# Kernel optimization log

Hardware: AMD Instinct MI355X
Metric: run time of the kernel (lower is better)

The kernel has to match this reference:

```python
import jax, jax.numpy as jnp
import numpy as np

N_NODES = 100000
N_EDGES = 1600000
DIM = 128
N_LAYERS = 4


def setup_inputs() -> dict:
    key = jax.random.key(0)
    ks = jax.random.split(key, 6)
    h = jax.random.normal(ks[0], (N_NODES, DIM), dtype=jnp.float32)
    src = jax.random.randint(ks[1], (N_EDGES,), 0, N_NODES, dtype=jnp.int32)
    dst = jax.random.randint(ks[2], (N_EDGES,), 0, N_NODES, dtype=jnp.int32)
    scale = 1.0 / np.sqrt(DIM)
    W_embed = jax.random.normal(ks[3], (DIM, DIM), dtype=jnp.float32) * scale
    b_embed = jnp.zeros((DIM,), dtype=jnp.float32)
    Ws = jax.random.normal(ks[4], (N_LAYERS, DIM, DIM), dtype=jnp.float32) * scale
    bs = jnp.zeros((N_LAYERS, DIM), dtype=jnp.float32)
    return {"h": h, "src": src, "dst": dst, "W_embed": W_embed,
            "b_embed": b_embed, "Ws": Ws, "bs": bs}


def reference(h, src, dst, W_embed, b_embed, Ws, bs):
    # Symmetric GCN normalization (DGL GraphConv norm='both'):
    # out-degree on src side, in-degree on dst side, clamped to >= 1.
    ones = jnp.ones(src.shape, h.dtype)
    deg_out = jax.ops.segment_sum(ones, src, num_segments=N_NODES)
    deg_in = jax.ops.segment_sum(ones, dst, num_segments=N_NODES)
    norm_s = jax.lax.rsqrt(jnp.maximum(deg_out, 1.0))  # [N]
    norm_d = jax.lax.rsqrt(jnp.maximum(deg_in, 1.0))   # [N]

    # embedding_h (dropout p=0 -> identity)
    h = h @ W_embed + b_embed

    for i in range(N_LAYERS):
        h_in = h
        # gather -> scale -> scatter-add (A_norm @ h)
        m = h[src] * norm_s[src, None]                              # [E, D]
        agg = jax.ops.segment_sum(m, dst, num_segments=N_NODES)    # [N, D]
        z = (agg * norm_d[:, None]) @ Ws[i] + bs[i]                 # GraphConv weight+bias
        z = jax.nn.relu(z)                                          # activation
        h = h_in + z                                                # residual
    return h
```

## Files before the change

### kernel.cpp

```cpp
#include <hip/hip_runtime.h>

#define DIMN 128
#define NLAYERS 4
#define KP 136
#define WTSH (2 * DIMN * KP)

#define BQL 9
#define BUCKW 512
#define BUCKCAP 10240
#define BSCH 4096
#define NBUK_MAX 256

#define HP_P 3
#define HP_C 48
#define HIST_BLOCKS (HP_P * HP_C)
#define HW_WORDS 16667

typedef __attribute__((ext_vector_type(8))) short bf16x8;
typedef __attribute__((ext_vector_type(4))) float f32x4;

__device__ inline float bfu2f(unsigned int u) { return __uint_as_float(u << 16); }
__device__ inline unsigned short f2bf(float f) {
    unsigned int u = __float_as_uint(f);
    return (unsigned short)((u + 0x7fffu + ((u >> 16) & 1u)) >> 16);
}
__device__ inline float blo(unsigned int u) { return __uint_as_float(u << 16); }
__device__ inline float bhi(unsigned int u) { return __uint_as_float(u & 0xffff0000u); }

__global__ __launch_bounds__(256) void k_pre(const int* __restrict__ src,
                                             const float* __restrict__ We,
                                             const float* __restrict__ Wlayers,
                                             unsigned int* __restrict__ degOutP,
                                             short* __restrict__ wt, int N, int E) {
    __shared__ unsigned int hsm[HW_WORDS];
    int tid = threadIdx.x;
    int bid = blockIdx.x;

    if (bid < HIST_BLOCKS) {
        int c = bid / HP_P;
        int p = bid % HP_P;
        int W = (N + 1) / 2;
        int w0 = p * HW_WORDS;
        int wn = min(HW_WORDS, W - w0);
        if (wn <= 0) return;
        int per = ((E + HP_C - 1) / HP_C + 3) & ~3;
        int e0 = c * per;
        int e1 = min(e0 + per, E);
        if (e0 >= e1) {
            for (int i = tid; i < wn; i += 256) degOutP[(size_t)c * W + w0 + i] = 0u;
            return;
        }
        for (int i = tid; i < wn; i += 256) hsm[i] = 0u;
        __syncthreads();
        int nvec = (e1 - e0) >> 2;
        const int4* sv = (const int4*)(src + e0);
        for (int it = tid; it < nvec; it += 256) {
            int4 v = sv[it];
            int w;
            w = (v.x >> 1) - w0; if ((unsigned)w < (unsigned)wn) atomicAdd(&hsm[w], 1u << ((v.x & 1) << 4));
            w = (v.y >> 1) - w0; if ((unsigned)w < (unsigned)wn) atomicAdd(&hsm[w], 1u << ((v.y & 1) << 4));
            w = (v.z >> 1) - w0; if ((unsigned)w < (unsigned)wn) atomicAdd(&hsm[w], 1u << ((v.z & 1) << 4));
            w = (v.w >> 1) - w0; if ((unsigned)w < (unsigned)wn) atomicAdd(&hsm[w], 1u << ((v.w & 1) << 4));
        }
        for (int j = e0 + (nvec << 2) + tid; j < e1; j += 256) {
            int s = src[j];
            int w = (s >> 1) - w0;
            if ((unsigned)w < (unsigned)wn) atomicAdd(&hsm[w], 1u << ((s & 1) << 4));
        }
        __syncthreads();
        for (int i = tid; i < wn; i += 256) degOutP[(size_t)c * W + w0 + i] = hsm[i];
        return;
    }

    {
        int m = bid - HIST_BLOCKS;
        const float* Wm = (m == 0) ? We : Wlayers + (size_t)(m - 1) * DIMN * DIMN;
        short* o = wt + (size_t)m * WTSH;
#pragma unroll
        for (int it = 0; it < 16; ++it) {
            int f = it * 1024 + tid * 4;
            float4 v = *(const float4*)(Wm + f);
            int k = f >> 7, n = f & 127;
            float vv[4] = {v.x, v.y, v.z, v.w};
#pragma unroll
            for (int j = 0; j < 4; ++j) {
                unsigned short hb = f2bf(vv[j]);
                float lo = vv[j] - bfu2f(hb);
                o[(n + j) * KP + k] = (short)hb;
                o[DIMN * KP + (n + j) * KP + k] = (short)f2bf(lo);
            }
        }
    }
}

__global__ __launch_bounds__(256) void k_binsort(const int* __restrict__ src,
                                                 const int* __restrict__ dst,
                                                 int* __restrict__ gcur,
                                                 int2* __restrict__ pairs,
                                                 int E, int NBUK) {
    __shared__ int cnt[NBUK_MAX];
    __shared__ int bofs[NBUK_MAX];
    __shared__ int gof[NBUK_MAX];
    __shared__ int scan_s[256];
    __shared__ int2 stg[BSCH];
    int tid = threadIdx.x;
    int e0 = blockIdx.x * BSCH;
    int n = min(BSCH, E - e0);
    if (n <= 0) return;
    cnt[tid] = 0;
    __syncthreads();

    int nv = n >> 2;
    const int4* dv4 = (const int4*)(dst + e0);
    for (int it = tid; it < nv; it += 256) {
        int4 d = dv4[it];
        atomicAdd(&cnt[d.x >> BQL], 1);
        atomicAdd(&cnt[d.y >> BQL], 1);
        atomicAdd(&cnt[d.z >> BQL], 1);
        atomicAdd(&cnt[d.w >> BQL], 1);
    }
    for (int j = (nv << 2) + tid; j < n; j += 256) {
        atomicAdd(&cnt[dst[e0 + j] >> BQL], 1);
    }
    __syncthreads();

    int myc = cnt[tid];
    scan_s[tid] = myc;
    __syncthreads();
    for (int off = 1; off < 256; off <<= 1) {
        int x = scan_s[tid];
        if (tid >= off) x += scan_s[tid - off];
        __syncthreads();
        scan_s[tid] = x;
        __syncthreads();
    }
    bofs[tid] = scan_s[tid] - myc;
    gof[tid] = (myc > 0 && tid < NBUK) ? atomicAdd(&gcur[tid], myc) : 0;
    cnt[tid] = 0;
    __syncthreads();

    const int4* sv4 = (const int4*)(src + e0);
    for (int it = tid; it < nv; it += 256) {
        int4 d = dv4[it];
        int4 s = sv4[it];
        int b, p;
        b = d.x >> BQL; p = bofs[b] + atomicAdd(&cnt[b], 1); stg[p] = make_int2(s.x, d.x);
        b = d.y >> BQL; p = bofs[b] + atomicAdd(&cnt[b], 1); stg[p] = make_int2(s.y, d.y);
        b = d.z >> BQL; p = bofs[b] + atomicAdd(&cnt[b], 1); stg[p] = make_int2(s.z, d.z);
        b = d.w >> BQL; p = bofs[b] + atomicAdd(&cnt[b], 1); stg[p] = make_int2(s.w, d.w);
    }
    for (int j = (nv << 2) + tid; j < n; j += 256) {
        int d = dst[e0 + j], s = src[e0 + j];
        int b = d >> BQL;
        int p = bofs[b] + atomicAdd(&cnt[b], 1);
        stg[p] = make_int2(s, d);
    }
    __syncthreads();

    for (int i = tid; i < n; i += 256) {
        int2 pr = stg[i];
        int b = pr.y >> BQL;
        int go = gof[b] + (i - bofs[b]);
        if (go < BUCKCAP) pairs[(size_t)b * BUCKCAP + go] = pr;
    }
}

__global__ __launch_bounds__(256) void k_build(const int2* __restrict__ pairs,
                                               const int* __restrict__ gcur,
                                               int* __restrict__ csr,
                                               int* __restrict__ rowptr,
                                               int* __restrict__ deg, int N) {
    int b = blockIdx.x;
    int tid = threadIdx.x;
    int cntb = gcur[b];
    if (cntb > BUCKCAP) cntb = BUCKCAP;
    __shared__ int c[BUCKW];
    __shared__ int pf[BUCKW];
    c[tid] = 0; c[tid + 256] = 0;
    __syncthreads();
    const int2* bp = pairs + (size_t)b * BUCKCAP;
    for (int i = tid; i < cntb; i += 256) atomicAdd(&c[bp[i].y & (BUCKW - 1)], 1);
    __syncthreads();
    pf[tid] = c[tid]; pf[tid + 256] = c[tid + 256];
    __syncthreads();
    for (int off = 1; off < BUCKW; off <<= 1) {
        int i0 = tid, i1 = tid + 256;
        int v0 = pf[i0] + ((i0 >= off) ? pf[i0 - off] : 0);
        int v1 = pf[i1] + ((i1 >= off) ? pf[i1 - off] : 0);
        __syncthreads();
        pf[i0] = v0; pf[i1] = v1;
        __syncthreads();
    }
    {
        int i0 = tid, i1 = tid + 256;
        int c0 = c[i0], c1 = c[i1];
        int ex0 = pf[i0] - c0, ex1 = pf[i1] - c1;
        pf[i0] = ex0; pf[i1] = ex1;
        int gn0 = (b << BQL) + i0, gn1 = (b << BQL) + i1;
        if (gn0 < N) { rowptr[gn0] = b * BUCKCAP + ex0; deg[gn0] = c0; }
        if (gn1 < N) { rowptr[gn1] = b * BUCKCAP + ex1; deg[gn1] = c1; }
        c[i0] = 0; c[i1] = 0;
    }
    __syncthreads();
    int* cb = csr + (size_t)b * BUCKCAP;
    for (int i = tid; i < cntb; i += 256) {
        int2 p = bp[i];
        int ld = p.y & (BUCKW - 1);
        int pos = pf[ld] + atomicAdd(&c[ld], 1);
        cb[pos] = p.x;
    }
}

__global__ __launch_bounds__(256) void k_norms(const int* __restrict__ deg,
                                               const unsigned int* __restrict__ degOutP,
                                               float* __restrict__ norm_d,
                                               float* __restrict__ norm_s, int N) {
    int i = blockIdx.x * 256 + threadIdx.x;
    int W = (N + 1) / 2;
    if (i < W) {
        unsigned s0 = 0, s1 = 0;
#pragma unroll 8
        for (int c = 0; c < HP_C; ++c) {
            unsigned v = degOutP[(size_t)c * W + i];
            s0 += v & 0xffffu;
            s1 += v >> 16;
        }
        int n0 = 2 * i, n1 = 2 * i + 1;
        norm_s[n0] = rsqrtf(fmaxf((float)s0, 1.0f));
        norm_d[n0] = rsqrtf(fmaxf((float)deg[n0], 1.0f));
        if (n1 < N) {
            norm_s[n1] = rsqrtf(fmaxf((float)s1, 1.0f));
            norm_d[n1] = rsqrtf(fmaxf((float)deg[n1], 1.0f));
        }
    }
}

__global__ __launch_bounds__(256) void k_gemm_f32(const float* __restrict__ A,
                                                  const short* __restrict__ Wt,
                                                  const float* __restrict__ bg,
                                                  float* __restrict__ tgt,
                                                  const float* __restrict__ norm_s,
                                                  unsigned short* __restrict__ Hs, int N) {
    __shared__ short Wl[WTSH];
    __shared__ float bias_s[DIMN];
    int tid = threadIdx.x;
    {
        const uint4* g = (const uint4*)Wt;
        uint4* l = (uint4*)Wl;
#pragma unroll
        for (int it = 0; it < 17; ++it) {
            int ix = it * 256 + tid;
            if (ix < WTSH / 8) l[ix] = g[ix];
        }
        if (tid < DIMN) bias_s[tid] = bg[tid];
    }
    __syncthreads();

    int lane = tid & 63;
    int wv = tid >> 6;
    int quad = lane >> 4;
    int l15 = lane & 15;
    int row0 = blockIdx.x * 128 + wv * 32;

    f32x4 acc[2][8];
#pragma unroll
    for (int s = 0; s < 2; ++s)
#pragma unroll
        for (int ct = 0; ct < 8; ++ct) acc[s][ct] = (f32x4){0.f, 0.f, 0.f, 0.f};

    for (int ks = 0; ks < 4; ++ks) {
        int kb = ks * 32 + quad * 8;
        bf16x8 ah[2], al[2];
#pragma unroll
        for (int s = 0; s < 2; ++s) {
            int r = row0 + s * 16 + l15;
            if (r > N - 1) r = N - 1;
            const float* ap = A + (size_t)r * DIMN + kb;
            float4 p = *(const float4*)ap;
            float4 q = *(const float4*)(ap + 4);
            float fv[8] = {p.x, p.y, p.z, p.w, q.x, q.y, q.z, q.w};
#pragma unroll
            for (int j = 0; j < 8; ++j) {
                unsigned short hb = f2bf(fv[j]);
                ah[s][j] = (short)hb;
                al[s][j] = (short)f2bf(fv[j] - bfu2f(hb));
            }
        }
#pragma unroll
        for (int ct = 0; ct < 8; ++ct) {
            const short* bp = Wl + (ct * 16 + l15) * KP + kb;
            bf16x8 bh = *(const bf16x8*)bp;
            bf16x8 bl = *(const bf16x8*)(bp + DIMN * KP);
#pragma unroll
            for (int s = 0; s < 2; ++s) {
                acc[s][ct] = __builtin_amdgcn_mfma_f32_16x16x32_bf16(ah[s], bh, acc[s][ct], 0, 0, 0);
                acc[s][ct] = __builtin_amdgcn_mfma_f32_16x16x32_bf16(al[s], bh, acc[s][ct], 0, 0, 0);
                acc[s][ct] = __builtin_amdgcn_mfma_f32_16x16x32_bf16(ah[s], bl, acc[s][ct], 0, 0, 0);
            }
        }
    }

#pragma unroll
    for (int s = 0; s < 2; ++s) {
        int rbase = row0 + s * 16 + quad * 4;
        float ns[4];
#pragma unroll
        for (int rj = 0; rj < 4; ++rj) {
            int row = rbase + rj;
            ns[rj] = (row < N) ? norm_s[row] : 0.f;
        }
#pragma unroll
        for (int ct = 0; ct < 8; ++ct) {
            int col = ct * 16 + l15;
            float bv = bias_s[col];
#pragma unroll
            for (int rj = 0; rj < 4; ++rj) {
                int row = rbase + rj;
                if (row < N) {
                    float o = acc[s][ct][rj] + bv;
                    __builtin_nontemporal_store(o, &tgt[(size_t)row * DIMN + col]);
                    Hs[(size_t)row * DIMN + col] = f2bf(o * ns[rj]);
                }
            }
        }
    }
}

__global__ __launch_bounds__(256) void k_gemm_bf(const unsigned short* __restrict__ A,
                                                 const short* __restrict__ Wt,
                                                 const float* __restrict__ bg,
                                                 const float* __restrict__ Hres,
                                                 float* __restrict__ tgt,
                                                 const float* __restrict__ norm_s,
                                                 unsigned short* __restrict__ Hs, int N) {
    __shared__ short Wl[WTSH];
    __shared__ float bias_s[DIMN];
    int tid = threadIdx.x;
    {
        const uint4* g = (const uint4*)Wt;
        uint4* l = (uint4*)Wl;
#pragma unroll
        for (int it = 0; it < 17; ++it) {
            int ix = it * 256 + tid;
            if (ix < WTSH / 8) l[ix] = g[ix];
        }
        if (tid < DIMN) bias_s[tid] = bg[tid];
    }
    __syncthreads();

    int lane = tid & 63;
    int wv = tid >> 6;
    int quad = lane >> 4;
    int l15 = lane & 15;
    int row0 = blockIdx.x * 128 + wv * 32;

    f32x4 acc[2][8];
#pragma unroll
    for (int s = 0; s < 2; ++s)
#pragma unroll
        for (int ct = 0; ct < 8; ++ct) acc[s][ct] = (f32x4){0.f, 0.f, 0.f, 0.f};

    for (int ks = 0; ks < 4; ++ks) {
        int kb = ks * 32 + quad * 8;
        bf16x8 ah[2];
#pragma unroll
        for (int s = 0; s < 2; ++s) {
            int r = row0 + s * 16 + l15;
            if (r > N - 1) r = N - 1;
            ah[s] = *(const bf16x8*)(A + (size_t)r * DIMN + kb);
        }
#pragma unroll
        for (int ct = 0; ct < 8; ++ct) {
            const short* bp = Wl + (ct * 16 + l15) * KP + kb;
            bf16x8 bh = *(const bf16x8*)bp;
            bf16x8 bl = *(const bf16x8*)(bp + DIMN * KP);
#pragma unroll
            for (int s = 0; s < 2; ++s) {
                acc[s][ct] = __builtin_amdgcn_mfma_f32_16x16x32_bf16(ah[s], bh, acc[s][ct], 0, 0, 0);
                acc[s][ct] = __builtin_amdgcn_mfma_f32_16x16x32_bf16(ah[s], bl, acc[s][ct], 0, 0, 0);
            }
        }
    }

    bool doHs = (Hs != nullptr);
#pragma unroll
    for (int s = 0; s < 2; ++s) {
        int rbase = row0 + s * 16 + quad * 4;
        float ns[4];
        if (doHs) {
#pragma unroll
            for (int rj = 0; rj < 4; ++rj) {
                int row = rbase + rj;
                ns[rj] = (row < N) ? norm_s[row] : 0.f;
            }
        }
#pragma unroll
        for (int ct = 0; ct < 8; ++ct) {
            int col = ct * 16 + l15;
            float bv = bias_s[col];
#pragma unroll
            for (int rj = 0; rj < 4; ++rj) {
                int row = rbase + rj;
                if (row < N) {
                    float o = fmaxf(acc[s][ct][rj] + bv, 0.f) + Hres[(size_t)row * DIMN + col];
                    __builtin_nontemporal_store(o, &tgt[(size_t)row * DIMN + col]);
                    if (doHs) Hs[(size_t)row * DIMN + col] = f2bf(o * ns[rj]);
                }
            }
        }
    }
}

__global__ __launch_bounds__(256) void k_spmm(const unsigned int* __restrict__ Hs,
                                              unsigned short* __restrict__ AggB,
                                              const int* __restrict__ csr,
                                              const int* __restrict__ rowptr,
                                              const int* __restrict__ deg,
                                              const float* __restrict__ norm_d, int N) {
    int wave = (blockIdx.x * blockDim.x + threadIdx.x) >> 6;
    int lane = threadIdx.x & 63;
    if (wave >= N) return;
    int cnt = deg[wave];
    const int* base = csr + rowptr[wave];
    int g = lane >> 5;
    int l5 = lane & 31;
    const uint2* H2 = (const uint2*)Hs;
    float4 acc = make_float4(0.f, 0.f, 0.f, 0.f);

    int emain = cnt & ~7;
    int e = 0;
    for (; e < emain; e += 8) {
        int s0 = base[e + g];
        int s1 = base[e + 2 + g];
        int s2 = base[e + 4 + g];
        int s3 = base[e + 6 + g];
        uint2 h0 = H2[(size_t)s0 * 32 + l5];
        uint2 h1 = H2[(size_t)s1 * 32 + l5];
        uint2 h2 = H2[(size_t)s2 * 32 + l5];
        uint2 h3 = H2[(size_t)s3 * 32 + l5];
        acc.x += blo(h0.x); acc.y += bhi(h0.x);
        acc.z += blo(h0.y); acc.w += bhi(h0.y);
        acc.x += blo(h1.x); acc.y += bhi(h1.x);
        acc.z += blo(h1.y); acc.w += bhi(h1.y);
        acc.x += blo(h2.x); acc.y += bhi(h2.x);
        acc.z += blo(h2.y); acc.w += bhi(h2.y);
        acc.x += blo(h3.x); acc.y += bhi(h3.x);
        acc.z += blo(h3.y); acc.w += bhi(h3.y);
    }
    for (; e < cnt; e += 2) {
        int ee = e + g;
        int sc = base[min(ee, cnt - 1)];
        uint2 hv = H2[(size_t)sc * 32 + l5];
        if (ee < cnt) {
            acc.x += blo(hv.x); acc.y += bhi(hv.x);
            acc.z += blo(hv.y); acc.w += bhi(hv.y);
        }
    }
    acc.x += __shfl_xor(acc.x, 32);
    acc.y += __shfl_xor(acc.y, 32);
    acc.z += __shfl_xor(acc.z, 32);
    acc.w += __shfl_xor(acc.w, 32);
    if (g == 0) {
        float nd = norm_d[wave];
        unsigned long long p =
            (unsigned long long)((unsigned)f2bf(acc.x * nd) | ((unsigned)f2bf(acc.y * nd) << 16)) |
            ((unsigned long long)((unsigned)f2bf(acc.z * nd) | ((unsigned)f2bf(acc.w * nd) << 16)) << 32);
        __builtin_nontemporal_store(p, &((unsigned long long*)AggB)[(size_t)wave * 32 + l5]);
    }
}

static inline char* align256(char* p) {
    return (char*)(((uintptr_t)p + 255) & ~(uintptr_t)255);
}

extern "C" void kernel_launch(void* const* d_in, const int* in_sizes, int n_in,
                              void* d_out, int out_size, void* d_ws, size_t ws_size,
                              hipStream_t stream) {
    const float* h_in = (const float*)d_in[0];
    const int* src = (const int*)d_in[1];
    const int* dst = (const int*)d_in[2];
    const float* W_embed = (const float*)d_in[3];
    const float* b_embed = (const float*)d_in[4];
    const float* Ws = (const float*)d_in[5];
    const float* bs = (const float*)d_in[6];
    float* out = (float*)d_out;

    const int N = in_sizes[0] / DIMN;
    const int E = in_sizes[1];
    const int W = (N + 1) / 2;
    const int NBUK = (N + BUCKW - 1) >> BQL;

    char* w = (char*)d_ws;
    float* Hc = (float*)w;               w = align256(w + (size_t)N * DIMN * 4);
    unsigned short* AggB = (unsigned short*)w; w = align256(w + (size_t)N * DIMN * 2);
    unsigned short* Hs = (unsigned short*)w;   w = align256(w + (size_t)N * DIMN * 2);
    int2* pairs = (int2*)w;              w = align256(w + (size_t)NBUK * BUCKCAP * 8);
    int* csr = (int*)w;                  w = align256(w + (size_t)NBUK * BUCKCAP * 4);
    int* rowptr = (int*)w;               w = align256(w + (size_t)N * 4);
    int* deg = (int*)w;                  w = align256(w + (size_t)N * 4);
    int* gcur = (int*)w;                 w = align256(w + (size_t)NBUK * 4);
    unsigned int* degOutP = (unsigned int*)w;  w = align256(w + (size_t)HP_C * W * 4);
    float* norm_s = (float*)w;           w = align256(w + (size_t)N * 4);
    float* norm_d = (float*)w;           w = align256(w + (size_t)N * 4);
    short* wt = (short*)w;               w = align256(w + (size_t)5 * WTSH * 2);

    (void)hipMemsetAsync(gcur, 0, (size_t)NBUK * 4, stream);

    int gb = (N + 127) / 128;
    int nb = (W + 255) / 256;
    int bb = (E + BSCH - 1) / BSCH;

    k_pre<<<HIST_BLOCKS + 5, 256, 0, stream>>>(src, W_embed, Ws, degOutP, wt, N, E);

    k_binsort<<<bb, 256, 0, stream>>>(src, dst, gcur, pairs, E, NBUK);
    k_build<<<NBUK, 256, 0, stream>>>(pairs, gcur, csr, rowptr, deg, N);

    k_norms<<<nb, 256, 0, stream>>>(deg, degOutP, norm_d, norm_s, N);

    k_gemm_f32<<<gb, 256, 0, stream>>>(h_in, wt, b_embed, Hc, norm_s, Hs, N);

    int sb = (N + 3) / 4;
    for (int l = 0; l < NLAYERS; ++l) {
        k_spmm<<<sb, 256, 0, stream>>>((const unsigned int*)Hs, AggB, csr, rowptr, deg, norm_d, N);
        float* tgt = (l == NLAYERS - 1) ? out : Hc;
        unsigned short* hs_next = (l == NLAYERS - 1) ? (unsigned short*)nullptr : Hs;
        k_gemm_bf<<<gb, 256, 0, stream>>>(AggB, wt + (size_t)(l + 1) * WTSH,
                                          bs + (size_t)l * DIMN, Hc, tgt, norm_s, hs_next, N);
    }
}
```

Before: 711.2 us.

## Read weights from global, stage GEMM epilogue through LDS for vectorized stores

The GEMM kernels no longer copy the split-bf16 weight matrices into shared memory; they read B fragments directly from global/L2 using an unpadded layout. The epilogue writes accumulators into a per-wave LDS buffer, then each lane writes a full row segment with float4 and uint4 stores, replacing scattered scalar stores. Launch bounds now request 4 blocks per SM, and the SpMM output store drops the nontemporal hint. The aim is to cut the per-block weight-staging cost and improve store coalescing. The risks are extra L2 traffic for weight reads, plus added block-level barriers in the epilogue.

```diff
diff --git a/kernel.cpp b/kernel.cpp
--- a/kernel.cpp
+++ b/kernel.cpp
@@ -2,8 +2,7 @@
 
 #define DIMN 128
 #define NLAYERS 4
-#define KP 136
-#define WTSH (2 * DIMN * KP)
+#define WTSH (2 * DIMN * DIMN)
 
 #define BQL 9
 #define BUCKW 512
@@ -23,6 +22,9 @@
 __device__ inline unsigned short f2bf(float f) {
     unsigned int u = __float_as_uint(f);
     return (unsigned short)((u + 0x7fffu + ((u >> 16) & 1u)) >> 16);
+}
+__device__ inline unsigned pack2(float a, float b) {
+    return (unsigned)f2bf(a) | ((unsigned)f2bf(b) << 16);
 }
 __device__ inline float blo(unsigned int u) { return __uint_as_float(u << 16); }
 __device__ inline float bhi(unsigned int u) { return __uint_as_float(u & 0xffff0000u); }
@@ -86,8 +88,8 @@
             for (int j = 0; j < 4; ++j) {
                 unsigned short hb = f2bf(vv[j]);
                 float lo = vv[j] - bfu2f(hb);
-                o[(n + j) * KP + k] = (short)hb;
-                o[DIMN * KP + (n + j) * KP + k] = (short)f2bf(lo);
+                o[(n + j) * DIMN + k] = (short)hb;
+                o[DIMN * DIMN + (n + j) * DIMN + k] = (short)f2bf(lo);
             }
         }
     }
@@ -235,25 +237,16 @@
     }
 }
 
-__global__ __launch_bounds__(256) void k_gemm_f32(const float* __restrict__ A,
-                                                  const short* __restrict__ Wt,
-                                                  const float* __restrict__ bg,
-                                                  float* __restrict__ tgt,
-                                                  const float* __restrict__ norm_s,
-                                                  unsigned short* __restrict__ Hs, int N) {
-    __shared__ short Wl[WTSH];
+__global__ __launch_bounds__(256, 4) void k_gemm_f32(const float* __restrict__ A,
+                                                     const short* __restrict__ Wt,
+                                                     const float* __restrict__ bg,
+                                                     float* __restrict__ tgt,
+                                                     const float* __restrict__ norm_s,
+                                                     unsigned short* __restrict__ Hs, int N) {
+    __shared__ __align__(16) float ebuf[4][16][132];
     __shared__ float bias_s[DIMN];
     int tid = threadIdx.x;
-    {
-        const uint4* g = (const uint4*)Wt;
-        uint4* l = (uint4*)Wl;
-#pragma unroll
-        for (int it = 0; it < 17; ++it) {
-            int ix = it * 256 + tid;
-            if (ix < WTSH / 8) l[ix] = g[ix];
-        }
-        if (tid < DIMN) bias_s[tid] = bg[tid];
-    }
+    if (tid < DIMN) bias_s[tid] = bg[tid];
     __syncthreads();
 
     int lane = tid & 63;
@@ -288,9 +281,9 @@
         }
 #pragma unroll
         for (int ct = 0; ct < 8; ++ct) {
-            const short* bp = Wl + (ct * 16 + l15) * KP + kb;
+            const short* bp = Wt + (ct * 16 + l15) * DIMN + kb;
             bf16x8 bh = *(const bf16x8*)bp;
-            bf16x8 bl = *(const bf16x8*)(bp + DIMN * KP);
+            bf16x8 bl = *(const bf16x8*)(bp + DIMN * DIMN);
 #pragma unroll
             for (int s = 0; s < 2; ++s) {
                 acc[s][ct] = __builtin_amdgcn_mfma_f32_16x16x32_bf16(ah[s], bh, acc[s][ct], 0, 0, 0);
@@ -300,52 +293,52 @@
         }
     }
 
+    float bv[8];
+#pragma unroll
+    for (int ct = 0; ct < 8; ++ct) bv[ct] = bias_s[ct * 16 + l15];
+
+    float (*eb)[132] = ebuf[wv];
+    int cg = lane >> 4;
 #pragma unroll
     for (int s = 0; s < 2; ++s) {
-        int rbase = row0 + s * 16 + quad * 4;
-        float ns[4];
-#pragma unroll
-        for (int rj = 0; rj < 4; ++rj) {
-            int row = rbase + rj;
-            ns[rj] = (row < N) ? norm_s[row] : 0.f;
-        }
-#pragma unroll
-        for (int ct = 0; ct < 8; ++ct) {
-            int col = ct * 16 + l15;
-            float bv = bias_s[col];
-#pragma unroll
-            for (int rj = 0; rj < 4; ++rj) {
-                int row = rbase + rj;
-                if (row < N) {
-                    float o = acc[s][ct][rj] + bv;
-                    __builtin_nontemporal_store(o, &tgt[(size_t)row * DIMN + col]);
-                    Hs[(size_t)row * DIMN + col] = f2bf(o * ns[rj]);
-                }
-            }
-        }
-    }
-}
-
-__global__ __launch_bounds__(256) void k_gemm_bf(const unsigned short* __restrict__ A,
-                                                 const short* __restrict__ Wt,
-                                                 const float* __restrict__ bg,
-                                                 const float* __restrict__ Hres,
-                                                 float* __restrict__ tgt,
-                                                 const float* __restrict__ norm_s,
-                                                 unsigned short* __restrict__ Hs, int N) {
-    __shared__ short Wl[WTSH];
+        __syncthreads();
+#pragma unroll
+        for (int ct = 0; ct < 8; ++ct)
+#pragma unroll
+            for (int rj = 0; rj < 4; ++rj)
+                eb[quad * 4 + rj][ct * 16 + l15] = acc[s][ct][rj] + bv[ct];
+        __syncthreads();
+        int row_g = row0 + s * 16 + l15;
+        if (row_g < N) {
+            float ns = norm_s[row_g];
+            float4* tp = (float4*)(tgt + (size_t)row_g * DIMN + cg * 32);
+            unsigned us[16];
+#pragma unroll
+            for (int k = 0; k < 8; ++k) {
+                float4 v = *(const float4*)&eb[l15][cg * 32 + k * 4];
+                tp[k] = v;
+                us[2 * k] = pack2(v.x * ns, v.y * ns);
+                us[2 * k + 1] = pack2(v.z * ns, v.w * ns);
+            }
+            uint4* hp = (uint4*)(Hs + (size_t)row_g * DIMN + cg * 32);
+#pragma unroll
+            for (int k4 = 0; k4 < 4; ++k4)
+                hp[k4] = make_uint4(us[4 * k4], us[4 * k4 + 1], us[4 * k4 + 2], us[4 * k4 + 3]);
+        }
+    }
+}
+
+__global__ __launch_bounds__(256, 4) void k_gemm_bf(const unsigned short* __restrict__ A,
+                                                    const short* __restrict__ Wt,
+                                                    const float* __restrict__ bg,
+                                                    const float* Hres,
+                                                    float* tgt,
+                                                    const float* __restrict__ norm_s,
+                                                    unsigned short* __restrict__ Hs, int N) {
+    __shared__ __align__(16) float ebuf[4][16][132];
     __shared__ float bias_s[DIMN];
     int tid = threadIdx.x;
-    {
-        const uint4* g = (const uint4*)Wt;
-        uint4* l = (uint4*)Wl;
-#pragma unroll
-        for (int it = 0; it < 17; ++it) {
-            int ix = it * 256 + tid;
-            if (ix < WTSH / 8) l[ix] = g[ix];
-        }
-        if (tid < DIMN) bias_s[tid] = bg[tid];
-    }
+    if (tid < DIMN) bias_s[tid] = bg[tid];
     __syncthreads();
 
     int lane = tid & 63;
@@ -371,9 +364,9 @@
         }
 #pragma unroll
         for (int ct = 0; ct < 8; ++ct) {
-            const short* bp = Wl + (ct * 16 + l15) * KP + kb;
+            const short* bp = Wt + (ct * 16 + l15) * DIMN + kb;
             bf16x8 bh = *(const bf16x8*)bp;
-            bf16x8 bl = *(const bf16x8*)(bp + DIMN * KP);
+            bf16x8 bl = *(const bf16x8*)(bp + DIMN * DIMN);
 #pragma unroll
             for (int s = 0; s < 2; ++s) {
                 acc[s][ct] = __builtin_amdgcn_mfma_f32_16x16x32_bf16(ah[s], bh, acc[s][ct], 0, 0, 0);
@@ -382,30 +375,46 @@
         }
     }
 
+    float bv[8];
+#pragma unroll
+    for (int ct = 0; ct < 8; ++ct) bv[ct] = bias_s[ct * 16 + l15];
+
     bool doHs = (Hs != nullptr);
+    float (*eb)[132] = ebuf[wv];
+    int cg = lane >> 4;
 #pragma unroll
     for (int s = 0; s < 2; ++s) {
-        int rbase = row0 + s * 16 + quad * 4;
-        float ns[4];
-        if (doHs) {
-#pragma unroll
-            for (int rj = 0; rj < 4; ++rj) {
-                int row = rbase + rj;
-                ns[rj] = (row < N) ? norm_s[row] : 0.f;
-            }
-        }
-#pragma unroll
-        for (int ct = 0; ct < 8; ++ct) {
-            int col = ct * 16 + l15;
-            float bv = bias_s[col];
-#pragma unroll
-            for (int rj = 0; rj < 4; ++rj) {
-                int row = rbase + rj;
-                if (row < N) {
-                    float o = fmaxf(acc[s][ct][rj] + bv, 0.f) + Hres[(size_t)row * DIMN + col];
-                    __builtin_nontemporal_store(o, &tgt[(size_t)row * DIMN + col]);
-                    if (doHs) Hs[(size_t)row * DIMN + col] = f2bf(o * ns[rj]);
-                }
+        __syncthreads();
+#pragma unroll
+        for (int ct = 0; ct < 8; ++ct)
+#pragma unroll
+            for (int rj = 0; rj < 4; ++rj)
+                eb[quad * 4 + rj][ct * 16 + l15] = acc[s][ct][rj] + bv[ct];
+        __syncthreads();
+        int row_g = row0 + s * 16 + l15;
+        if (row_g < N) {
+            float ns = doHs ? norm_s[row_g] : 0.f;
+            const float4* rp = (const float4*)(Hres + (size_t)row_g * DIMN + cg * 32);
+            float4* tp = (float4*)(tgt + (size_t)row_g * DIMN + cg * 32);
+            unsigned us[16];
+#pragma unroll
+            for (int k = 0; k < 8; ++k) {
+                float4 v = *(const float4*)&eb[l15][cg * 32 + k * 4];
+                float4 h = rp[k];
+                float4 o;
+                o.x = fmaxf(v.x, 0.f) + h.x;
+                o.y = fmaxf(v.y, 0.f) + h.y;
+                o.z = fmaxf(v.z, 0.f) + h.z;
+                o.w = fmaxf(v.w, 0.f) + h.w;
+                tp[k] = o;
+                us[2 * k] = pack2(o.x * ns, o.y * ns);
+                us[2 * k + 1] = pack2(o.z * ns, o.w * ns);
+            }
+            if (doHs) {
+                uint4* hp = (uint4*)(Hs + (size_t)row_g * DIMN + cg * 32);
+#pragma unroll
+                for (int k4 = 0; k4 < 4; ++k4)
+                    hp[k4] = make_uint4(us[4 * k4], us[4 * k4 + 1], us[4 * k4 + 2], us[4 * k4 + 3]);
             }
         }
     }
@@ -465,7 +474,7 @@
         unsigned long long p =
             (unsigned long long)((unsigned)f2bf(acc.x * nd) | ((unsigned)f2bf(acc.y * nd) << 16)) |
             ((unsigned long long)((unsigned)f2bf(acc.z * nd) | ((unsigned)f2bf(acc.w * nd) << 16)) << 32);
-        __builtin_nontemporal_store(p, &((unsigned long long*)AggB)[(size_t)wave * 32 + l5]);
+        ((unsigned long long*)AggB)[(size_t)wave * 32 + l5] = p;
     }
 }
 
```

Measured after the change: 856.7 us. 1.2x slower.

## Stage GEMM epilogue through LDS for vectorized row stores and prefetch A rows

Applied to the files above, without the earlier changes.

Both GEMM kernels now load all of a lane's A fragments up front, before the MFMA loop, and fully unroll the k loop. The epilogue now writes accumulators into LDS (reusing the weight buffer after a barrier), so each lane then owns a contiguous 32-column slice of one row. That lets the fp32 output, the residual input and the bf16 scaled copy use 16-byte vector loads and stores instead of scattered scalar 4-byte and 2-byte accesses. The cost is an extra LDS round trip, a barrier and higher register pressure from the prefetched fragments.

```diff
diff --git a/kernel.cpp b/kernel.cpp
--- a/kernel.cpp
+++ b/kernel.cpp
@@ -23,6 +23,9 @@
 __device__ inline unsigned short f2bf(float f) {
     unsigned int u = __float_as_uint(f);
     return (unsigned short)((u + 0x7fffu + ((u >> 16) & 1u)) >> 16);
+}
+__device__ inline unsigned pack2(float a, float b) {
+    return (unsigned)f2bf(a) | ((unsigned)f2bf(b) << 16);
 }
 __device__ inline float blo(unsigned int u) { return __uint_as_float(u << 16); }
 __device__ inline float bhi(unsigned int u) { return __uint_as_float(u & 0xffff0000u); }
@@ -241,7 +244,7 @@
                                                   float* __restrict__ tgt,
                                                   const float* __restrict__ norm_s,
                                                   unsigned short* __restrict__ Hs, int N) {
-    __shared__ short Wl[WTSH];
+    __shared__ __align__(16) short Wl[WTSH];
     __shared__ float bias_s[DIMN];
     int tid = threadIdx.x;
     {
@@ -262,22 +265,33 @@
     int l15 = lane & 15;
     int row0 = blockIdx.x * 128 + wv * 32;
 
+    float4 af[4][2][2];
+#pragma unroll
+    for (int s = 0; s < 2; ++s) {
+        int r = row0 + s * 16 + l15;
+        if (r > N - 1) r = N - 1;
+        const float* ap = A + (size_t)r * DIMN + quad * 8;
+#pragma unroll
+        for (int ks = 0; ks < 4; ++ks) {
+            af[ks][s][0] = *(const float4*)(ap + ks * 32);
+            af[ks][s][1] = *(const float4*)(ap + ks * 32 + 4);
+        }
+    }
+
     f32x4 acc[2][8];
 #pragma unroll
     for (int s = 0; s < 2; ++s)
 #pragma unroll
         for (int ct = 0; ct < 8; ++ct) acc[s][ct] = (f32x4){0.f, 0.f, 0.f, 0.f};
 
+#pragma unroll
     for (int ks = 0; ks < 4; ++ks) {
         int kb = ks * 32 + quad * 8;
         bf16x8 ah[2], al[2];
 #pragma unroll
         for (int s = 0; s < 2; ++s) {
-            int r = row0 + s * 16 + l15;
-            if (r > N - 1) r = N - 1;
-            const float* ap = A + (size_t)r * DIMN + kb;
-            float4 p = *(const float4*)ap;
-            float4 q = *(const float4*)(ap + 4);
+            float4 p = af[ks][s][0];
+            float4 q = af[ks][s][1];
             float fv[8] = {p.x, p.y, p.z, p.w, q.x, q.y, q.z, q.w};
 #pragma unroll
             for (int j = 0; j < 8; ++j) {
@@ -300,28 +314,36 @@
         }
     }
 
+    float bv[8];
+#pragma unroll
+    for (int ct = 0; ct < 8; ++ct) bv[ct] = bias_s[ct * 16 + l15];
+
+    __syncthreads();
+    float (*eb)[132] = (float (*)[132])Wl + wv * 16;
 #pragma unroll
     for (int s = 0; s < 2; ++s) {
-        int rbase = row0 + s * 16 + quad * 4;
-        float ns[4];
-#pragma unroll
-        for (int rj = 0; rj < 4; ++rj) {
-            int row = rbase + rj;
-            ns[rj] = (row < N) ? norm_s[row] : 0.f;
-        }
-#pragma unroll
-        for (int ct = 0; ct < 8; ++ct) {
-            int col = ct * 16 + l15;
-            float bv = bias_s[col];
-#pragma unroll
-            for (int rj = 0; rj < 4; ++rj) {
-                int row = rbase + rj;
-                if (row < N) {
-                    float o = acc[s][ct][rj] + bv;
-                    __builtin_nontemporal_store(o, &tgt[(size_t)row * DIMN + col]);
-                    Hs[(size_t)row * DIMN + col] = f2bf(o * ns[rj]);
-                }
-            }
+        int row_g = row0 + s * 16 + l15;
+        bool rowok = (row_g < N);
+#pragma unroll
+        for (int ct = 0; ct < 8; ++ct)
+#pragma unroll
+            for (int rj = 0; rj < 4; ++rj)
+                eb[quad * 4 + rj][ct * 16 + l15] = acc[s][ct][rj] + bv[ct];
+        if (rowok) {
+            float ns = norm_s[row_g];
+            float* tp = tgt + (size_t)row_g * DIMN + quad * 32;
+            unsigned us[16];
+#pragma unroll
+            for (int k = 0; k < 8; ++k) {
+                f32x4 v = *(const f32x4*)&eb[l15][quad * 32 + k * 4];
+                __builtin_nontemporal_store(v, (f32x4*)(tp + k * 4));
+                us[2 * k] = pack2(v[0] * ns, v[1] * ns);
+                us[2 * k + 1] = pack2(v[2] * ns, v[3] * ns);
+            }
+            uint4* hp = (uint4*)(Hs + (size_t)row_g * DIMN + quad * 32);
+#pragma unroll
+            for (int k4 = 0; k4 < 4; ++k4)
+                hp[k4] = make_uint4(us[4 * k4], us[4 * k4 + 1], us[4 * k4 + 2], us[4 * k4 + 3]);
         }
     }
 }
@@ -333,7 +355,7 @@
                                                  float* __restrict__ tgt,
                                                  const float* __restrict__ norm_s,
                                                  unsigned short* __restrict__ Hs, int N) {
-    __shared__ short Wl[WTSH];
+    __shared__ __align__(16) short Wl[WTSH];
     __shared__ float bias_s[DIMN];
     int tid = threadIdx.x;
     {
@@ -354,21 +376,26 @@
     int l15 = lane & 15;
     int row0 = blockIdx.x * 128 + wv * 32;
 
+    bf16x8 ahh[4][2];
+#pragma unroll
+    for (int s = 0; s < 2; ++s) {
+        int r = row0 + s * 16 + l15;
+        if (r > N - 1) r = N - 1;
+        const unsigned short* ap = A + (size_t)r * DIMN + quad * 8;
+#pragma unroll
+        for (int ks = 0; ks < 4; ++ks)
+            ahh[ks][s] = *(const bf16x8*)(ap + ks * 32);
+    }
+
     f32x4 acc[2][8];
 #pragma unroll
     for (int s = 0; s < 2; ++s)
 #pragma unroll
         for (int ct = 0; ct < 8; ++ct) acc[s][ct] = (f32x4){0.f, 0.f, 0.f, 0.f};
 
+#pragma unroll
     for (int ks = 0; ks < 4; ++ks) {
         int kb = ks * 32 + quad * 8;
-        bf16x8 ah[2];
-#pragma unroll
-        for (int s = 0; s < 2; ++s) {
-            int r = row0 + s * 16 + l15;
-            if (r > N - 1) r = N - 1;
-            ah[s] = *(const bf16x8*)(A + (size_t)r * DIMN + kb);
-        }
 #pragma unroll
         for (int ct = 0; ct < 8; ++ct) {
             const short* bp = Wl + (ct * 16 + l15) * KP + kb;
@@ -376,36 +403,55 @@
             bf16x8 bl = *(const bf16x8*)(bp + DIMN * KP);
 #pragma unroll
             for (int s = 0; s < 2; ++s) {
-                acc[s][ct] = __builtin_amdgcn_mfma_f32_16x16x32_bf16(ah[s], bh, acc[s][ct], 0, 0, 0);
-                acc[s][ct] = __builtin_amdgcn_mfma_f32_16x16x32_bf16(ah[s], bl, acc[s][ct], 0, 0, 0);
-            }
-        }
-    }
+                acc[s][ct] = __builtin_amdgcn_mfma_f32_16x16x32_bf16(ahh[ks][s], bh, acc[s][ct], 0, 0, 0);
+                acc[s][ct] = __builtin_amdgcn_mfma_f32_16x16x32_bf16(ahh[ks][s], bl, acc[s][ct], 0, 0, 0);
+            }
+        }
+    }
+
+    float bv[8];
+#pragma unroll
+    for (int ct = 0; ct < 8; ++ct) bv[ct] = bias_s[ct * 16 + l15];
 
     bool doHs = (Hs != nullptr);
+    __syncthreads();
+    float (*eb)[132] = (float (*)[132])Wl + wv * 16;
 #pragma unroll
     for (int s = 0; s < 2; ++s) {
-        int rbase = row0 + s * 16 + quad * 4;
-        float ns[4];
-        if (doHs) {
-#pragma unroll
-            for (int rj = 0; rj < 4; ++rj) {
-                int row = rbase + rj;
-                ns[rj] = (row < N) ? norm_s[row] : 0.f;
-            }
-        }
-#pragma unroll
-        for (int ct = 0; ct < 8; ++ct) {
-            int col = ct * 16 + l15;
-            float bv = bias_s[col];
-#pragma unroll
-            for (int rj = 0; rj < 4; ++rj) {
-                int row = rbase + rj;
-                if (row < N) {
-                    float o = fmaxf(acc[s][ct][rj] + bv, 0.f) + Hres[(size_t)row * DIMN + col];
-                    __builtin_nontemporal_store(o, &tgt[(size_t)row * DIMN + col]);
-                    if (doHs) Hs[(size_t)row * DIMN + col] = f2bf(o * ns[rj]);
-                }
+        int row_g = row0 + s * 16 + l15;
+        bool rowok = (row_g < N);
+        float4 h[8];
+        if (rowok) {
+            const float4* rp = (const float4*)(Hres + (size_t)row_g * DIMN + quad * 32);
+#pragma unroll
+            for (int k = 0; k < 8; ++k) h[k] = rp[k];
+        }
+#pragma unroll
+        for (int ct = 0; ct < 8; ++ct)
+#pragma unroll
+            for (int rj = 0; rj < 4; ++rj)
+                eb[quad * 4 + rj][ct * 16 + l15] = acc[s][ct][rj] + bv[ct];
+        if (rowok) {
+            float ns = doHs ? norm_s[row_g] : 0.f;
+            float* tp = tgt + (size_t)row_g * DIMN + quad * 32;
+            unsigned us[16];
+#pragma unroll
+            for (int k = 0; k < 8; ++k) {
+                f32x4 v = *(const f32x4*)&eb[l15][quad * 32 + k * 4];
+                f32x4 o;
+                o[0] = fmaxf(v[0], 0.f) + h[k].x;
+                o[1] = fmaxf(v[1], 0.f) + h[k].y;
+                o[2] = fmaxf(v[2], 0.f) + h[k].z;
+                o[3] = fmaxf(v[3], 0.f) + h[k].w;
+                __builtin_nontemporal_store(o, (f32x4*)(tp + k * 4));
+                us[2 * k] = pack2(o[0] * ns, o[1] * ns);
+                us[2 * k + 1] = pack2(o[2] * ns, o[3] * ns);
+            }
+            if (doHs) {
+                uint4* hp = (uint4*)(Hs + (size_t)row_g * DIMN + quad * 32);
+#pragma unroll
+                for (int k4 = 0; k4 < 4; ++k4)
+                    hp[k4] = make_uint4(us[4 * k4], us[4 * k4 + 1], us[4 * k4 + 2], us[4 * k4 + 3]);
             }
         }
     }
```

Result: slower. 825.3 us (+16.0%).
